# Optimization experiments

Hardware: AMD Instinct MI355X
Metric: run time of the kernel (lower is better)

## Reference

```python
import jax, jax.numpy as jnp
import numpy as np

N_ITERS = 10
LAMBDA0 = 0.01


def skew(p):
    # p: (..., 3) -> (..., 3, 3) skew-symmetric matrices
    x, y, z = p[..., 0], p[..., 1], p[..., 2]
    O = jnp.zeros_like(x)
    return jnp.stack([O, -z, y, z, O, -x, -y, x, O], -1).reshape(p.shape[:-1] + (3, 3))


def so3exp(w):
    # Rodrigues formula for a single (3,) rotation vector
    theta2 = jnp.sum(w * w)
    theta = jnp.sqrt(theta2 + 1e-24)
    small = theta < 1e-4
    a = jnp.where(small, 1.0 - theta2 / 6.0, jnp.sin(theta) / theta)
    b = jnp.where(small, 0.5 - theta2 / 24.0, (1.0 - jnp.cos(theta)) / (theta2 + 1e-24))
    W = skew(w)
    return jnp.eye(3, dtype=w.dtype) + a * W + b * (W @ W)


def gather_feats(fm, p2, width, height):
    # fm: (C, Hf, Wf); p2: (N, 2) int pixel coords (x, y). Mirrors indexing_ with
    # flipped points: row = floor(y*Hf/height), col = floor(x*Wf/width).
    Hf, Wf = fm.shape[1], fm.shape[2]
    rows = jnp.clip((p2[:, 1] * Hf) // height, 0, Hf - 1)
    cols = jnp.clip((p2[:, 0] * Wf) // width, 0, Wf - 1)
    return fm[:, rows, cols].T  # (N, C)


def project(pts3D, R, t, K):
    p3 = pts3D @ R.T + t                                  # (N, 3) camera frame
    proj = p3 @ K.T
    xy = jnp.clip(proj[:, :2] / proj[:, 2:3], -1e6, 1e6)  # from_homogeneous
    p2 = jnp.round(xy).astype(jnp.int32) - 1              # (N, 2) int pixels
    return p3, p2


def support_mask(p2, width, height):
    return (p2[:, 0] >= 0) & (p2[:, 1] >= 0) & (p2[:, 0] < width) & (p2[:, 1] < height)


def masked_mean_cost(fm, feature_ref, p2, mask, width, height):
    err = gather_feats(fm, p2, width, height) - feature_ref
    m = mask.astype(err.dtype)
    c = 0.5 * jnp.sum(err * err, -1) * m
    return jnp.sum(c) / jnp.maximum(jnp.sum(m), 1.0)


def setup_inputs():
    key = jax.random.key(0)
    ks = jax.random.split(key, 7)
    N, C, Hf, Wf = 50000, 128, 480, 640
    z = jax.random.uniform(ks[0], (N,), minval=4.0, maxval=8.0)
    x = jax.random.uniform(ks[1], (N,), minval=-0.4, maxval=0.4) * z
    y = jax.random.uniform(ks[2], (N,), minval=-0.3, maxval=0.3) * z
    pts3D = jnp.stack([x, y, z], -1).astype(jnp.float32)
    feature_map_query = jax.random.normal(ks[3], (C, Hf, Wf), jnp.float32)
    feature_grad_x = 0.1 * jax.random.normal(ks[4], (C, Hf, Wf), jnp.float32)
    feature_grad_y = 0.1 * jax.random.normal(ks[5], (C, Hf, Wf), jnp.float32)
    feature_ref = jax.random.normal(ks[6], (N, C), jnp.float32)
    K = jnp.array([[600.0, 0.0, 320.0], [0.0, 600.0, 240.0], [0.0, 0.0, 1.0]], jnp.float32)
    R_init = jnp.eye(3, dtype=jnp.float32)
    t_init = jnp.array([0.1, 0.1, 0.0], jnp.float32)
    return dict(pts3D=pts3D, feature_ref=feature_ref, feature_map_query=feature_map_query,
                feature_grad_x=feature_grad_x, feature_grad_y=feature_grad_y, K=K,
                R_init=R_init, t_init=t_init, im_width=640, im_height=480)


def reference(pts3D, feature_ref, feature_map_query, feature_grad_x, feature_grad_y,
              K, R_init, t_init, im_width, im_height):
    N = pts3D.shape[0]
    fx, fy = K[0, 0], K[1, 1]
    R, t = R_init, t_init
    lam = jnp.asarray(LAMBDA0, pts3D.dtype)
    lr = jnp.asarray(1.0, pts3D.dtype)
    lr_reset = 1.0

    # initial cost (prev_cost at iteration 0 in the original)
    _, p2_0 = project(pts3D, R, t, K)
    mask0 = support_mask(p2_0, im_width, im_height)
    prev_cost = masked_mean_cost(feature_map_query, feature_ref, p2_0, mask0, im_width, im_height)

    eyeN = jnp.broadcast_to(jnp.eye(3, dtype=pts3D.dtype), (N, 3, 3))

    for _ in range(N_ITERS):
        p3, p2 = project(pts3D, R, t, K)
        mask = support_mask(p2, im_width, im_height)
        m = mask.astype(pts3D.dtype)

        err = gather_feats(feature_map_query, p2, im_width, im_height) - feature_ref  # (N, C)

        Z = p3[:, 2]
        Zs = jnp.where(jnp.abs(Z) > 1e-6, Z, 1e-6)  # guard masked-out points only
        # J_p_T: d p3 / d [t, w]  -> (N, 3, 6)
        J_p_T = jnp.concatenate([eyeN, -skew(p3)], -1)
        o = jnp.ones_like(Zs)
        zz = jnp.zeros_like(Zs)
        # J_px_p: d pixel / d p3 -> (N, 2, 3)
        J_px_p = jnp.stack([fx * o, zz, -fx * p3[:, 0] / Zs,
                            zz, fy * o, -fy * p3[:, 1] / Zs], -1).reshape(N, 2, 3) / Zs[:, None, None]
        gx = gather_feats(feature_grad_x, p2, im_width, im_height)  # (N, C)
        gy = gather_feats(feature_grad_y, p2, im_width, im_height)
        J_f_px = jnp.stack([gx, gy], -1)            # (N, C, 2)
        J = J_f_px @ (J_px_p @ J_p_T)               # (N, C, 6)
        Jm = J * m[:, None, None]                   # zero out unsupported points

        Grad = jnp.einsum('ncj,nc->j', Jm, err)     # (6,)
        Hess = jnp.einsum('nck,ncl->kl', Jm, Jm)    # (6, 6)

        Hd = Hess + lam * jnp.diag(jnp.diagonal(Hess) + 1e-9)
        delta = -lr * (jnp.linalg.inv(Hd) @ Grad)
        dt, dw = delta[:3], delta[3:6]
        dr = so3exp(dw)
        R_new = dr @ R
        t_new = dr @ t + dt

        _, p2n = project(pts3D, R_new, t_new, K)
        maskn = support_mask(p2n, im_width, im_height)
        new_cost = masked_mean_cost(feature_map_query, feature_ref, p2n, maskn, im_width, im_height)

        accept = new_cost <= prev_cost
        lam = jnp.clip(lam * jnp.where(accept, 0.1, 10.0), 1e-6, 1e4)
        lr = jnp.where(accept, lr_reset, jnp.clip(0.1 * lr, 1e-3, 1.0))
        R = jnp.where(accept, R_new, R)
        t = jnp.where(accept, t_new, t)
        prev_cost = jnp.where(accept, new_cost, prev_cost)

    return R, t
```

## Files before the change

### kernel.cpp

```cpp
#include <hip/hip_runtime.h>
#include <math.h>

#define NCH 128
#define IMW 640
#define IMH 480
#define HW (IMW * IMH)
#define THREADS 512
#define WPB (THREADS / 64)
#define GBLK 512
#define TSTRIDE (3 * NCH)

#define S_R    0
#define S_T    9
#define S_RC   12
#define S_TC   21
#define S_LAM  24
#define S_LR   25
#define S_PREV 26
#define S_G    32
#define S_TOTAL 64

#define PCOLS 29

__device__ __forceinline__ float sel6(int k, float v0, float v1, float v2,
                                      float v3, float v4, float v5) {
  float r = v0;
  r = (k == 1) ? v1 : r;
  r = (k == 2) ? v2 : r;
  r = (k == 3) ? v3 : r;
  r = (k == 4) ? v4 : r;
  r = (k == 5) ? v5 : r;
  return r;
}

struct ProjR {
  float x, y, z;
  int pix;
  bool m;
};

__device__ __forceinline__ ProjR project_pt(const float* __restrict__ pts, int n,
                                            const float R[9], const float T[3],
                                            const float Kv[9]) {
  float px = pts[3 * n + 0], py = pts[3 * n + 1], pz = pts[3 * n + 2];
  ProjR o;
  o.x = R[0] * px + R[1] * py + R[2] * pz + T[0];
  o.y = R[3] * px + R[4] * py + R[5] * pz + T[1];
  o.z = R[6] * px + R[7] * py + R[8] * pz + T[2];
  float pr0 = Kv[0] * o.x + Kv[1] * o.y + Kv[2] * o.z;
  float pr1 = Kv[3] * o.x + Kv[4] * o.y + Kv[5] * o.z;
  float pr2 = Kv[6] * o.x + Kv[7] * o.y + Kv[8] * o.z;
  float u = fminf(fmaxf(pr0 / pr2, -1000000.0f), 1000000.0f);
  float v = fminf(fmaxf(pr1 / pr2, -1000000.0f), 1000000.0f);
  int p2x = (int)rintf(u) - 1;
  int p2y = (int)rintf(v) - 1;
  o.m = (p2x >= 0) && (p2y >= 0) && (p2x < IMW) && (p2y < IMH);
  int r = min(max(p2y, 0), IMH - 1);
  int c = min(max(p2x, 0), IMW - 1);
  o.pix = r * IMW + c;
  return o;
}

__device__ __forceinline__ void jac_rows(const ProjR& p, float fx, float fy,
                                         float A0[6], float A1[6]) {
  float Zs = (fabsf(p.z) > 1e-6f) ? p.z : 1e-6f;
  float iz = 1.0f / Zs;
  float j00 = fx * iz;
  float j02 = -fx * p.x * iz * iz;
  float j11 = fy * iz;
  float j12 = -fy * p.y * iz * iz;
  A0[0] = j00; A0[1] = 0.0f; A0[2] = j02;
  A0[3] = j02 * p.y; A0[4] = j00 * p.z - j02 * p.x; A0[5] = -j00 * p.y;
  A1[0] = 0.0f; A1[1] = j11; A1[2] = j12;
  A1[3] = -j11 * p.z + j12 * p.y; A1[4] = -j12 * p.x; A1[5] = j11 * p.x;
}

__global__ void init_kernel(const float* __restrict__ Rin,
                            const float* __restrict__ tin,
                            double* __restrict__ st) {
  int i = threadIdx.x;
  if (i < 9) { st[S_R + i] = (double)Rin[i]; st[S_RC + i] = (double)Rin[i]; }
  if (i < 3) { st[S_T + i] = (double)tin[i]; st[S_TC + i] = (double)tin[i]; }
  if (i == 0) { st[S_LAM] = 0.01; st[S_LR] = 1.0; st[S_PREV] = 0.0; }
}

__global__ __launch_bounds__(256) void transpose3_kernel(
    const float* __restrict__ f, const float* __restrict__ gx,
    const float* __restrict__ gy, float* __restrict__ t) {
  __shared__ float tile[64][NCH + 1];
  const int map = blockIdx.y;
  const float* in = (map == 0) ? f : (map == 1) ? gx : gy;
  const int pix0 = blockIdx.x * 64;
  for (int k = threadIdx.x; k < 64 * NCH / 4; k += 256) {
    int c = k >> 4;
    int p4 = (k & 15) * 4;
    float4 v = ((const float4*)(in + (size_t)c * HW + pix0))[k & 15];
    tile[p4 + 0][c] = v.x;
    tile[p4 + 1][c] = v.y;
    tile[p4 + 2][c] = v.z;
    tile[p4 + 3][c] = v.w;
  }
  __syncthreads();
  for (int k = threadIdx.x; k < 64 * NCH / 4; k += 256) {
    int px = k >> 5;
    int c4 = (k & 31) * 4;
    float4 v = make_float4(tile[px][c4], tile[px][c4 + 1], tile[px][c4 + 2],
                           tile[px][c4 + 3]);
    ((float4*)(t + (size_t)(pix0 + px) * TSTRIDE + (size_t)map * NCH))[k & 31] = v;
  }
}

template <bool TRANS>
__global__ __launch_bounds__(THREADS) void fused_kernel(
    const float* __restrict__ pts, const float* __restrict__ fref,
    const float* __restrict__ mf, const float* __restrict__ mgx,
    const float* __restrict__ mgy, const float* __restrict__ Kmat,
    const double* __restrict__ st, double* __restrict__ part, int N) {
  const int lane = threadIdx.x & 63;
  const int wib = threadIdx.x >> 6;
  const int gw = blockIdx.x * WPB + wib;
  const int nw = gridDim.x * WPB;

  float R[9], T[3], Kv[9];
#pragma unroll
  for (int i = 0; i < 9; ++i) { R[i] = (float)st[S_RC + i]; Kv[i] = Kmat[i]; }
#pragma unroll
  for (int i = 0; i < 3; ++i) T[i] = (float)st[S_TC + i];
  const float fx = Kv[0], fy = Kv[4];

  int kq = 0, lq = 0;
  if (lane < 6) {
    kq = lane; lq = lane;
  } else if (lane < 27) {
    int q = lane - 6, k = 0;
    while (q >= 6 - k) { q -= 6 - k; ++k; }
    kq = k; lq = k + q;
  }

  double acc = 0.0, csum = 0.0, cnt = 0.0;

  for (int n = gw; n < N; n += nw) {
    ProjR p = project_pt(pts, n, R, T, Kv);
    if (!p.m) continue;
    float A0[6], A1[6];
    jac_rows(p, fx, fy, A0, A1);

    float e0, e1, gx0, gx1, gy0, gy1;
    if (TRANS) {
      const size_t base = (size_t)p.pix * TSTRIDE + 2 * lane;
      float2 f  = *(const float2*)(mf + base);
      float2 gx = *(const float2*)(mf + base + NCH);
      float2 gy = *(const float2*)(mf + base + 2 * NCH);
      float2 fr = *(const float2*)(fref + (size_t)n * NCH + 2 * lane);
      e0 = f.x - fr.x; e1 = f.y - fr.y;
      gx0 = gx.x; gx1 = gx.y; gy0 = gy.x; gy1 = gy.y;
    } else {
      const size_t base = (size_t)p.pix;
      const int c0 = lane, c1 = lane + 64;
      float f0 = mf[(size_t)c0 * HW + base], f1 = mf[(size_t)c1 * HW + base];
      gx0 = mgx[(size_t)c0 * HW + base]; gx1 = mgx[(size_t)c1 * HW + base];
      gy0 = mgy[(size_t)c0 * HW + base]; gy1 = mgy[(size_t)c1 * HW + base];
      float r0 = fref[(size_t)n * NCH + c0], r1 = fref[(size_t)n * NCH + c1];
      e0 = f0 - r0; e1 = f1 - r1;
    }

    csum += (double)(e0 * e0 + e1 * e1);
    if (lane == 0) cnt += 1.0;

    float sxx = gx0 * gx0 + gx1 * gx1;
    float sxy = gx0 * gy0 + gx1 * gy1;
    float syy = gy0 * gy0 + gy1 * gy1;
    float sxe = gx0 * e0 + gx1 * e1;
    float sye = gy0 * e0 + gy1 * e1;
#pragma unroll
    for (int off = 32; off > 0; off >>= 1) {
      sxx += __shfl_xor(sxx, off);
      sxy += __shfl_xor(sxy, off);
      syy += __shfl_xor(syy, off);
      sxe += __shfl_xor(sxe, off);
      sye += __shfl_xor(sye, off);
    }
    float a0k = sel6(kq, A0[0], A0[1], A0[2], A0[3], A0[4], A0[5]);
    float a1k = sel6(kq, A1[0], A1[1], A1[2], A1[3], A1[4], A1[5]);
    float a0l = sel6(lq, A0[0], A0[1], A0[2], A0[3], A0[4], A0[5]);
    float a1l = sel6(lq, A1[0], A1[1], A1[2], A1[3], A1[4], A1[5]);
    float contrib;
    if (lane < 6)
      contrib = sxe * a0k + sye * a1k;
    else
      contrib = sxx * a0k * a0l + sxy * (a0k * a1l + a1k * a0l) +
                syy * a1k * a1l;
    if (lane < 27) acc += (double)contrib;
  }

#pragma unroll
  for (int off = 32; off > 0; off >>= 1) {
    csum += __shfl_xor(csum, off);
    cnt += __shfl_xor(cnt, off);
  }

  __shared__ double red[WPB][PCOLS];
  if (lane < 27) red[wib][lane] = acc;
  if (lane == 0) { red[wib][27] = csum; red[wib][28] = cnt; }
  __syncthreads();
  if (wib == 0 && lane < PCOLS) {
    double s = 0.0;
#pragma unroll
    for (int w = 0; w < WPB; ++w) s += red[w][lane];
    part[(size_t)blockIdx.x * PCOLS + lane] = s;
  }
}

__global__ void update_solve_kernel(const double* __restrict__ part, int GB,
                                    double* __restrict__ st,
                                    float* __restrict__ out, int is_init) {
  __shared__ double red[16][PCOLS];
  __shared__ double tot[PCOLS];
  int q = threadIdx.x & 31;
  int chunk = threadIdx.x >> 5;
  if (q < PCOLS) {
    double s = 0.0;
    for (int b = chunk; b < GB; b += 16) s += part[(size_t)b * PCOLS + q];
    red[chunk][q] = s;
  }
  __syncthreads();
  if (threadIdx.x < PCOLS) {
    double t = 0.0;
#pragma unroll
    for (int ch = 0; ch < 16; ++ch) t += red[ch][threadIdx.x];
    tot[threadIdx.x] = t;
  }
  __syncthreads();
  if (threadIdx.x == 0) {
    double nc = 0.5 * tot[27] / fmax(tot[28], 1.0);
    bool accept;
    if (is_init) {
      accept = true;
      st[S_PREV] = nc;
    } else {
      accept = (nc <= st[S_PREV]);
      double lam = st[S_LAM] * (accept ? 0.1 : 10.0);
      st[S_LAM] = fmin(fmax(lam, 1e-6), 1e4);
      st[S_LR] = accept ? 1.0 : fmin(fmax(0.1 * st[S_LR], 1e-3), 1.0);
      if (accept) st[S_PREV] = nc;
    }
    if (accept) {
      for (int i = 0; i < 9; ++i) st[S_R + i] = st[S_RC + i];
      for (int i = 0; i < 3; ++i) st[S_T + i] = st[S_TC + i];
      for (int j = 0; j < 27; ++j) st[S_G + j] = tot[j];
    }
    for (int i = 0; i < 9; ++i) out[i] = (float)st[S_R + i];
    for (int i = 0; i < 3; ++i) out[9 + i] = (float)st[S_T + i];

    double Grad[6], Hs[6][6];
    for (int j = 0; j < 6; ++j) Grad[j] = st[S_G + j];
    int qq = 0;
    for (int k = 0; k < 6; ++k)
      for (int l = k; l < 6; ++l) { Hs[k][l] = Hs[l][k] = st[S_G + 6 + qq]; ++qq; }
    double lam = st[S_LAM], lr = st[S_LR];
    double M[6][7];
    for (int i = 0; i < 6; ++i) {
      for (int j = 0; j < 6; ++j) M[i][j] = Hs[i][j];
      M[i][i] += lam * (Hs[i][i] + 1e-9);
      M[i][6] = Grad[i];
    }
    for (int c = 0; c < 6; ++c) {
      int piv = c;
      double mx = fabs(M[c][c]);
      for (int r = c + 1; r < 6; ++r) {
        double a = fabs(M[r][c]);
        if (a > mx) { mx = a; piv = r; }
      }
      if (piv != c)
        for (int j = 0; j < 7; ++j) {
          double tmp = M[c][j]; M[c][j] = M[piv][j]; M[piv][j] = tmp;
        }
      double pv = M[c][c];
      if (pv == 0.0) pv = 1e-30;
      for (int r = c + 1; r < 6; ++r) {
        double f = M[r][c] / pv;
        for (int j = c; j < 7; ++j) M[r][j] -= f * M[c][j];
      }
    }
    double xs[6];
    for (int i = 5; i >= 0; --i) {
      double v = M[i][6];
      for (int j = i + 1; j < 6; ++j) v -= M[i][j] * xs[j];
      double pv = M[i][i];
      if (pv == 0.0) pv = 1e-30;
      xs[i] = v / pv;
    }
    double dt[3] = {-lr * xs[0], -lr * xs[1], -lr * xs[2]};
    double dw[3] = {-lr * xs[3], -lr * xs[4], -lr * xs[5]};
    double th2 = dw[0] * dw[0] + dw[1] * dw[1] + dw[2] * dw[2];
    double th = sqrt(th2 + 1e-24);
    double a, b;
    if (th < 1e-4) { a = 1.0 - th2 / 6.0; b = 0.5 - th2 / 24.0; }
    else { a = sin(th) / th; b = (1.0 - cos(th)) / (th2 + 1e-24); }
    double W[3][3] = {{0, -dw[2], dw[1]}, {dw[2], 0, -dw[0]}, {-dw[1], dw[0], 0}};
    double W2[3][3];
    for (int i = 0; i < 3; ++i)
      for (int j = 0; j < 3; ++j) {
        double s = 0.0;
        for (int k = 0; k < 3; ++k) s += W[i][k] * W[k][j];
        W2[i][j] = s;
      }
    double dr[3][3];
    for (int i = 0; i < 3; ++i)
      for (int j = 0; j < 3; ++j)
        dr[i][j] = ((i == j) ? 1.0 : 0.0) + a * W[i][j] + b * W2[i][j];
    for (int i = 0; i < 3; ++i) {
      for (int j = 0; j < 3; ++j) {
        double s = 0.0;
        for (int k = 0; k < 3; ++k) s += dr[i][k] * st[S_R + k * 3 + j];
        st[S_RC + i * 3 + j] = s;
      }
      double s = 0.0;
      for (int k = 0; k < 3; ++k) s += dr[i][k] * st[S_T + k];
      st[S_TC + i] = s + dt[i];
    }
  }
}

extern "C" void kernel_launch(void* const* d_in, const int* in_sizes, int n_in,
                              void* d_out, int out_size, void* d_ws, size_t ws_size,
                              hipStream_t stream) {
  const float* pts  = (const float*)d_in[0];
  const float* fref = (const float*)d_in[1];
  const float* fm   = (const float*)d_in[2];
  const float* gxm  = (const float*)d_in[3];
  const float* gym  = (const float*)d_in[4];
  const float* Kmat = (const float*)d_in[5];
  const float* Rin  = (const float*)d_in[6];
  const float* tin  = (const float*)d_in[7];
  const int N = in_sizes[0] / 3;

  double* st = (double*)d_ws;
  double* part = st + S_TOTAL;
  float* out = (float*)d_out;

  const size_t state_doubles = S_TOTAL + (size_t)GBLK * PCOLS;
  const size_t map_floats = (size_t)HW * NCH;
  const size_t need_fast =
      state_doubles * sizeof(double) + 3 * map_floats * sizeof(float) + 256;

  init_kernel<<<1, 64, 0, stream>>>(Rin, tin, st);

  if (ws_size >= need_fast) {
    float* tmap = (float*)(st + state_doubles);
    transpose3_kernel<<<dim3(HW / 64, 3), 256, 0, stream>>>(fm, gxm, gym, tmap);
    fused_kernel<true><<<GBLK, THREADS, 0, stream>>>(pts, fref, tmap, tmap, tmap,
                                                     Kmat, st, part, N);
    update_solve_kernel<<<1, 512, 0, stream>>>(part, GBLK, st, out, 1);
    for (int it = 0; it < 10; ++it) {
      fused_kernel<true><<<GBLK, THREADS, 0, stream>>>(pts, fref, tmap, tmap,
                                                       tmap, Kmat, st, part, N);
      update_solve_kernel<<<1, 512, 0, stream>>>(part, GBLK, st, out, 0);
    }
  } else {
    fused_kernel<false><<<GBLK, THREADS, 0, stream>>>(pts, fref, fm, gxm, gym,
                                                      Kmat, st, part, N);
    update_solve_kernel<<<1, 512, 0, stream>>>(part, GBLK, st, out, 1);
    for (int it = 0; it < 10; ++it) {
      fused_kernel<false><<<GBLK, THREADS, 0, stream>>>(pts, fref, fm, gxm, gym,
                                                        Kmat, st, part, N);
      update_solve_kernel<<<1, 512, 0, stream>>>(part, GBLK, st, out, 0);
    }
  }
}
```

Baseline: 957.6 us.

## Process two points per wavefront with float4 loads and per-lane Hessian accumulators

The fused Gauss-Newton kernel now handles two points per 64-lane wavefront, one per half-wave, with each lane loading float4 channel chunks. Each lane keeps all 27 Hessian and gradient terms in float registers and reduces them once after the loop, which removes the per-point cross-lane shuffle reductions and the sel6 selects. The transpose kernel switches to an XOR-swizzled float4 shared-memory tile with unrolled loops to avoid bank conflicts. The cost is higher register pressure from the 27 accumulators and float rather than double accumulation for the Hessian inside each lane.

```diff
diff --git a/kernel.cpp b/kernel.cpp
--- a/kernel.cpp
+++ b/kernel.cpp
@@ -21,17 +21,6 @@
 #define S_TOTAL 64
 
 #define PCOLS 29
-
-__device__ __forceinline__ float sel6(int k, float v0, float v1, float v2,
-                                      float v3, float v4, float v5) {
-  float r = v0;
-  r = (k == 1) ? v1 : r;
-  r = (k == 2) ? v2 : r;
-  r = (k == 3) ? v3 : r;
-  r = (k == 4) ? v4 : r;
-  r = (k == 5) ? v5 : r;
-  return r;
-}
 
 struct ProjR {
   float x, y, z;
@@ -87,26 +76,31 @@
 __global__ __launch_bounds__(256) void transpose3_kernel(
     const float* __restrict__ f, const float* __restrict__ gx,
     const float* __restrict__ gy, float* __restrict__ t) {
-  __shared__ float tile[64][NCH + 1];
+  __shared__ float4 tile4[64][32];
   const int map = blockIdx.y;
   const float* in = (map == 0) ? f : (map == 1) ? gx : gy;
   const int pix0 = blockIdx.x * 64;
-  for (int k = threadIdx.x; k < 64 * NCH / 4; k += 256) {
-    int c = k >> 4;
+#pragma unroll
+  for (int mm = 0; mm < 8; ++mm) {
+    int k = threadIdx.x + 256 * mm;
+    int c  = k >> 4;
     int p4 = (k & 15) * 4;
     float4 v = ((const float4*)(in + (size_t)c * HW + pix0))[k & 15];
-    tile[p4 + 0][c] = v.x;
-    tile[p4 + 1][c] = v.y;
-    tile[p4 + 2][c] = v.z;
-    tile[p4 + 3][c] = v.w;
+    int sw = (c >> 2) ^ (k & 15);
+    int e  = c & 3;
+    ((float*)&tile4[p4 + 0][sw])[e] = v.x;
+    ((float*)&tile4[p4 + 1][sw])[e] = v.y;
+    ((float*)&tile4[p4 + 2][sw])[e] = v.z;
+    ((float*)&tile4[p4 + 3][sw])[e] = v.w;
   }
   __syncthreads();
-  for (int k = threadIdx.x; k < 64 * NCH / 4; k += 256) {
+#pragma unroll
+  for (int mm = 0; mm < 8; ++mm) {
+    int k = threadIdx.x + 256 * mm;
     int px = k >> 5;
-    int c4 = (k & 31) * 4;
-    float4 v = make_float4(tile[px][c4], tile[px][c4 + 1], tile[px][c4 + 2],
-                           tile[px][c4 + 3]);
-    ((float4*)(t + (size_t)(pix0 + px) * TSTRIDE + (size_t)map * NCH))[k & 31] = v;
+    int c4 = k & 31;
+    float4 v = tile4[px][c4 ^ (px >> 2)];
+    ((float4*)(t + (size_t)(pix0 + px) * TSTRIDE + (size_t)map * NCH))[c4] = v;
   }
 }
 
@@ -117,9 +111,11 @@
     const float* __restrict__ mgy, const float* __restrict__ Kmat,
     const double* __restrict__ st, double* __restrict__ part, int N) {
   const int lane = threadIdx.x & 63;
-  const int wib = threadIdx.x >> 6;
+  const int wib  = threadIdx.x >> 6;
   const int gw = blockIdx.x * WPB + wib;
   const int nw = gridDim.x * WPB;
+  const int half = lane >> 5;
+  const int hl   = lane & 31;
 
   float R[9], T[3], Kv[9];
 #pragma unroll
@@ -128,80 +124,101 @@
   for (int i = 0; i < 3; ++i) T[i] = (float)st[S_TC + i];
   const float fx = Kv[0], fy = Kv[4];
 
-  int kq = 0, lq = 0;
-  if (lane < 6) {
-    kq = lane; lq = lane;
-  } else if (lane < 27) {
-    int q = lane - 6, k = 0;
-    while (q >= 6 - k) { q -= 6 - k; ++k; }
-    kq = k; lq = k + q;
-  }
-
-  double acc = 0.0, csum = 0.0, cnt = 0.0;
-
-  for (int n = gw; n < N; n += nw) {
-    ProjR p = project_pt(pts, n, R, T, Kv);
-    if (!p.m) continue;
+  float hacc[27];
+#pragma unroll
+  for (int j = 0; j < 27; ++j) hacc[j] = 0.0f;
+  double csum = 0.0;
+  float cntf = 0.0f;
+
+  for (int base = gw * 2; base < N; base += 2 * nw) {
+    const int n = base + half;
+    const int nc = min(n, N - 1);
+    ProjR p = project_pt(pts, nc, R, T, Kv);
+    const float m = (p.m && n < N) ? 1.0f : 0.0f;
+    if (__all(m == 0.0f)) continue;
+
     float A0[6], A1[6];
     jac_rows(p, fx, fy, A0, A1);
 
-    float e0, e1, gx0, gx1, gy0, gy1;
+    float e0, e1, e2, e3;
+    float gxx, gxy, gyy, gxe, gye;
     if (TRANS) {
-      const size_t base = (size_t)p.pix * TSTRIDE + 2 * lane;
-      float2 f  = *(const float2*)(mf + base);
-      float2 gx = *(const float2*)(mf + base + NCH);
-      float2 gy = *(const float2*)(mf + base + 2 * NCH);
-      float2 fr = *(const float2*)(fref + (size_t)n * NCH + 2 * lane);
-      e0 = f.x - fr.x; e1 = f.y - fr.y;
-      gx0 = gx.x; gx1 = gx.y; gy0 = gy.x; gy1 = gy.y;
+      const float4* t4 = (const float4*)mf;
+      const size_t b = (size_t)p.pix * (TSTRIDE / 4) + hl;
+      float4 fv = t4[b];
+      float4 gv = t4[b + 32];
+      float4 hv = t4[b + 64];
+      float4 rv = ((const float4*)fref)[(size_t)nc * (NCH / 4) + hl];
+      e0 = fv.x - rv.x; e1 = fv.y - rv.y; e2 = fv.z - rv.z; e3 = fv.w - rv.w;
+      gxx = gv.x * gv.x + gv.y * gv.y + gv.z * gv.z + gv.w * gv.w;
+      gxy = gv.x * hv.x + gv.y * hv.y + gv.z * hv.z + gv.w * hv.w;
+      gyy = hv.x * hv.x + hv.y * hv.y + hv.z * hv.z + hv.w * hv.w;
+      gxe = gv.x * e0 + gv.y * e1 + gv.z * e2 + gv.w * e3;
+      gye = hv.x * e0 + hv.y * e1 + hv.z * e2 + hv.w * e3;
     } else {
-      const size_t base = (size_t)p.pix;
-      const int c0 = lane, c1 = lane + 64;
-      float f0 = mf[(size_t)c0 * HW + base], f1 = mf[(size_t)c1 * HW + base];
-      gx0 = mgx[(size_t)c0 * HW + base]; gx1 = mgx[(size_t)c1 * HW + base];
-      gy0 = mgy[(size_t)c0 * HW + base]; gy1 = mgy[(size_t)c1 * HW + base];
-      float r0 = fref[(size_t)n * NCH + c0], r1 = fref[(size_t)n * NCH + c1];
-      e0 = f0 - r0; e1 = f1 - r1;
-    }
-
-    csum += (double)(e0 * e0 + e1 * e1);
-    if (lane == 0) cnt += 1.0;
-
-    float sxx = gx0 * gx0 + gx1 * gx1;
-    float sxy = gx0 * gy0 + gx1 * gy1;
-    float syy = gy0 * gy0 + gy1 * gy1;
-    float sxe = gx0 * e0 + gx1 * e1;
-    float sye = gy0 * e0 + gy1 * e1;
+      const int c0 = hl * 4;
+      const size_t bb = (size_t)p.pix;
+      float f0 = mf[(size_t)(c0 + 0) * HW + bb];
+      float f1 = mf[(size_t)(c0 + 1) * HW + bb];
+      float f2 = mf[(size_t)(c0 + 2) * HW + bb];
+      float f3 = mf[(size_t)(c0 + 3) * HW + bb];
+      float gx0 = mgx[(size_t)(c0 + 0) * HW + bb];
+      float gx1 = mgx[(size_t)(c0 + 1) * HW + bb];
+      float gx2 = mgx[(size_t)(c0 + 2) * HW + bb];
+      float gx3 = mgx[(size_t)(c0 + 3) * HW + bb];
+      float gy0 = mgy[(size_t)(c0 + 0) * HW + bb];
+      float gy1 = mgy[(size_t)(c0 + 1) * HW + bb];
+      float gy2 = mgy[(size_t)(c0 + 2) * HW + bb];
+      float gy3 = mgy[(size_t)(c0 + 3) * HW + bb];
+      float4 rv = ((const float4*)fref)[(size_t)nc * (NCH / 4) + hl];
+      e0 = f0 - rv.x; e1 = f1 - rv.y; e2 = f2 - rv.z; e3 = f3 - rv.w;
+      gxx = gx0 * gx0 + gx1 * gx1 + gx2 * gx2 + gx3 * gx3;
+      gxy = gx0 * gy0 + gx1 * gy1 + gx2 * gy2 + gx3 * gy3;
+      gyy = gy0 * gy0 + gy1 * gy1 + gy2 * gy2 + gy3 * gy3;
+      gxe = gx0 * e0 + gx1 * e1 + gx2 * e2 + gx3 * e3;
+      gye = gy0 * e0 + gy1 * e1 + gy2 * e2 + gy3 * e3;
+    }
+
+    gxx *= m; gxy *= m; gyy *= m; gxe *= m; gye *= m;
+    csum += (double)(m * (e0 * e0 + e1 * e1 + e2 * e2 + e3 * e3));
+    if (hl == 0) cntf += m;
+
+#pragma unroll
+    for (int k = 0; k < 6; ++k) hacc[k] += gxe * A0[k] + gye * A1[k];
+    float u[6], v[6];
+#pragma unroll
+    for (int k = 0; k < 6; ++k) {
+      u[k] = gxx * A0[k] + gxy * A1[k];
+      v[k] = gxy * A0[k] + gyy * A1[k];
+    }
+    int q = 6;
+#pragma unroll
+    for (int k = 0; k < 6; ++k)
+#pragma unroll
+      for (int l = k; l < 6; ++l) {
+        hacc[q] += u[k] * A0[l] + v[k] * A1[l];
+        ++q;
+      }
+  }
+
+  __shared__ double red[WPB][PCOLS];
+#pragma unroll
+  for (int j = 0; j < 27; ++j) {
+    double d = (double)hacc[j];
+#pragma unroll
+    for (int off = 32; off > 0; off >>= 1) d += __shfl_xor(d, off);
+    if (lane == 0) red[wib][j] = d;
+  }
+  {
+    double cs = csum;
+    float cf = cntf;
 #pragma unroll
     for (int off = 32; off > 0; off >>= 1) {
-      sxx += __shfl_xor(sxx, off);
-      sxy += __shfl_xor(sxy, off);
-      syy += __shfl_xor(syy, off);
-      sxe += __shfl_xor(sxe, off);
-      sye += __shfl_xor(sye, off);
-    }
-    float a0k = sel6(kq, A0[0], A0[1], A0[2], A0[3], A0[4], A0[5]);
-    float a1k = sel6(kq, A1[0], A1[1], A1[2], A1[3], A1[4], A1[5]);
-    float a0l = sel6(lq, A0[0], A0[1], A0[2], A0[3], A0[4], A0[5]);
-    float a1l = sel6(lq, A1[0], A1[1], A1[2], A1[3], A1[4], A1[5]);
-    float contrib;
-    if (lane < 6)
-      contrib = sxe * a0k + sye * a1k;
-    else
-      contrib = sxx * a0k * a0l + sxy * (a0k * a1l + a1k * a0l) +
-                syy * a1k * a1l;
-    if (lane < 27) acc += (double)contrib;
-  }
-
-#pragma unroll
-  for (int off = 32; off > 0; off >>= 1) {
-    csum += __shfl_xor(csum, off);
-    cnt += __shfl_xor(cnt, off);
-  }
-
-  __shared__ double red[WPB][PCOLS];
-  if (lane < 27) red[wib][lane] = acc;
-  if (lane == 0) { red[wib][27] = csum; red[wib][28] = cnt; }
+      cs += __shfl_xor(cs, off);
+      cf += __shfl_xor(cf, off);
+    }
+    if (lane == 0) { red[wib][27] = cs; red[wib][28] = (double)cf; }
+  }
   __syncthreads();
   if (wib == 0 && lane < PCOLS) {
     double s = 0.0;
```

After: 1.033 ms. +7.9%, slower.

## Sort points by initial projected pixel bucket and retile the feature-map transpose

Applied to the files above, without the earlier changes.

Adds a counting sort of the points by their initial projected pixel (in buckets of 64 pixels) and permutes the points and reference features into that order. Later gathers from the transposed feature maps then hit nearby memory. The transpose kernel is also rewritten to use 32-pixel tiles, 512 threads, all three maps per block, and a swizzled float4 shared layout to avoid bank conflicts. In exchange it adds five extra kernels, an atomic scatter and more workspace. The locality gain relies on the pose staying close to the initial one across iterations.

```diff
diff --git a/kernel.cpp b/kernel.cpp
--- a/kernel.cpp
+++ b/kernel.cpp
@@ -9,6 +9,9 @@
 #define WPB (THREADS / 64)
 #define GBLK 512
 #define TSTRIDE (3 * NCH)
+#define TPX 32
+#define NTILE (HW / TPX)
+#define NBUCK (HW / 64)
 
 #define S_R    0
 #define S_T    9
@@ -77,36 +80,131 @@
 
 __global__ void init_kernel(const float* __restrict__ Rin,
                             const float* __restrict__ tin,
-                            double* __restrict__ st) {
-  int i = threadIdx.x;
-  if (i < 9) { st[S_R + i] = (double)Rin[i]; st[S_RC + i] = (double)Rin[i]; }
-  if (i < 3) { st[S_T + i] = (double)tin[i]; st[S_TC + i] = (double)tin[i]; }
-  if (i == 0) { st[S_LAM] = 0.01; st[S_LR] = 1.0; st[S_PREV] = 0.0; }
-}
-
-__global__ __launch_bounds__(256) void transpose3_kernel(
+                            double* __restrict__ st, int* __restrict__ hist) {
+  if (blockIdx.x == 0) {
+    int i = threadIdx.x;
+    if (i < 9) { st[S_R + i] = (double)Rin[i]; st[S_RC + i] = (double)Rin[i]; }
+    if (i < 3) { st[S_T + i] = (double)tin[i]; st[S_TC + i] = (double)tin[i]; }
+    if (i == 0) { st[S_LAM] = 0.01; st[S_LR] = 1.0; st[S_PREV] = 0.0; }
+  }
+  int gid = blockIdx.x * blockDim.x + threadIdx.x;
+  for (int i = gid; i < NBUCK; i += gridDim.x * blockDim.x) hist[i] = 0;
+}
+
+__global__ __launch_bounds__(256) void sort_key_kernel(
+    const float* __restrict__ pts, const float* __restrict__ Rin,
+    const float* __restrict__ tin, const float* __restrict__ Kmat,
+    int* __restrict__ keys, int* __restrict__ hist, int N) {
+  int n = blockIdx.x * 256 + threadIdx.x;
+  if (n >= N) return;
+  float R[9], T[3], Kv[9];
+#pragma unroll
+  for (int i = 0; i < 9; ++i) { R[i] = Rin[i]; Kv[i] = Kmat[i]; }
+#pragma unroll
+  for (int i = 0; i < 3; ++i) T[i] = tin[i];
+  ProjR p = project_pt(pts, n, R, T, Kv);
+  keys[n] = p.pix;
+  atomicAdd(&hist[p.pix >> 6], 1);
+}
+
+__global__ __launch_bounds__(512) void sort_scan_kernel(
+    const int* __restrict__ hist, int* __restrict__ offs) {
+  __shared__ int tsum[512];
+  const int C = (NBUCK + 511) / 512;
+  int t = threadIdx.x;
+  int local[C];
+  int s = 0;
+#pragma unroll
+  for (int j = 0; j < C; ++j) {
+    int idx = t * C + j;
+    int v = (idx < NBUCK) ? hist[idx] : 0;
+    local[j] = s;
+    s += v;
+  }
+  tsum[t] = s;
+  __syncthreads();
+  for (int off = 1; off < 512; off <<= 1) {
+    int y = (t >= off) ? tsum[t - off] : 0;
+    __syncthreads();
+    tsum[t] += y;
+    __syncthreads();
+  }
+  int base = (t == 0) ? 0 : tsum[t - 1];
+#pragma unroll
+  for (int j = 0; j < C; ++j) {
+    int idx = t * C + j;
+    if (idx < NBUCK) offs[idx] = base + local[j];
+  }
+}
+
+__global__ __launch_bounds__(256) void sort_scatter_kernel(
+    const int* __restrict__ keys, int* __restrict__ offs,
+    int* __restrict__ order, int N) {
+  int n = blockIdx.x * 256 + threadIdx.x;
+  if (n >= N) return;
+  int b = keys[n] >> 6;
+  int pos = atomicAdd(&offs[b], 1);
+  order[pos] = n;
+}
+
+__global__ __launch_bounds__(256) void permute_kernel(
+    const float* __restrict__ pts, const float* __restrict__ fref,
+    const int* __restrict__ order, float* __restrict__ pts_s,
+    float* __restrict__ fref_s, int N) {
+  int gid = blockIdx.x * 256 + threadIdx.x;
+  int tot4 = N * (NCH / 4);
+  for (int idx = gid; idx < tot4; idx += gridDim.x * 256) {
+    int i = idx >> 5, c4 = idx & 31;
+    int n = order[i];
+    ((float4*)fref_s)[(size_t)i * 32 + c4] =
+        ((const float4*)fref)[(size_t)n * 32 + c4];
+  }
+  int tot3 = N * 3;
+  for (int idx = gid; idx < tot3; idx += gridDim.x * 256) {
+    int i = idx / 3, r = idx - i * 3;
+    pts_s[idx] = pts[3 * order[i] + r];
+  }
+}
+
+__global__ __launch_bounds__(512) void transpose3_kernel(
     const float* __restrict__ f, const float* __restrict__ gx,
     const float* __restrict__ gy, float* __restrict__ t) {
-  __shared__ float tile[64][NCH + 1];
-  const int map = blockIdx.y;
-  const float* in = (map == 0) ? f : (map == 1) ? gx : gy;
-  const int pix0 = blockIdx.x * 64;
-  for (int k = threadIdx.x; k < 64 * NCH / 4; k += 256) {
-    int c = k >> 4;
-    int p4 = (k & 15) * 4;
-    float4 v = ((const float4*)(in + (size_t)c * HW + pix0))[k & 15];
-    tile[p4 + 0][c] = v.x;
-    tile[p4 + 1][c] = v.y;
-    tile[p4 + 2][c] = v.z;
-    tile[p4 + 3][c] = v.w;
+  __shared__ float4 l4[TPX * 96];
+  const int bx = blockIdx.x;
+  const int tile = (bx & 7) * (NTILE / 8) + (bx >> 3);
+  const int pix0 = tile * TPX;
+
+  float4 v[6];
+#pragma unroll
+  for (int it = 0; it < 6; ++it) {
+    int k = threadIdx.x + 512 * it;
+    int map = k >> 10;
+    int r = k & 1023;
+    int c = r >> 3;
+    int g = r & 7;
+    const float* in = (map == 0) ? f : (map == 1) ? gx : gy;
+    v[it] = ((const float4*)(in + (size_t)c * HW + pix0))[g];
+  }
+#pragma unroll
+  for (int it = 0; it < 6; ++it) {
+    int k = threadIdx.x + 512 * it;
+    int map = k >> 10;
+    int r = k & 1023;
+    int c = r >> 3, g = r & 7;
+    int j = map * 32 + (c >> 2), e = c & 3;
+    int jb = j ^ g;
+    ((float*)&l4[(4 * g + 0) * 96 + (jb ^ 0)])[e] = v[it].x;
+    ((float*)&l4[(4 * g + 1) * 96 + (jb ^ 1)])[e] = v[it].y;
+    ((float*)&l4[(4 * g + 2) * 96 + (jb ^ 2)])[e] = v[it].z;
+    ((float*)&l4[(4 * g + 3) * 96 + (jb ^ 3)])[e] = v[it].w;
   }
   __syncthreads();
-  for (int k = threadIdx.x; k < 64 * NCH / 4; k += 256) {
-    int px = k >> 5;
-    int c4 = (k & 31) * 4;
-    float4 v = make_float4(tile[px][c4], tile[px][c4 + 1], tile[px][c4 + 2],
-                           tile[px][c4 + 3]);
-    ((float4*)(t + (size_t)(pix0 + px) * TSTRIDE + (size_t)map * NCH))[k & 31] = v;
+#pragma unroll
+  for (int it = 0; it < 6; ++it) {
+    int o = threadIdx.x + 512 * it;
+    int px = o / 96, j = o % 96;
+    float4 w = l4[px * 96 + (j ^ ((px >> 2) & 7) ^ (px & 3))];
+    ((float4*)t)[(size_t)pix0 * 96 + o] = w;
   }
 }
 
@@ -337,20 +435,48 @@
 
   double* st = (double*)d_ws;
   double* part = st + S_TOTAL;
+  int* keys  = (int*)(part + (size_t)GBLK * PCOLS);
+  int* order = keys + N;
+  int* hist  = order + N;
+  int* offs  = hist + NBUCK;
+  size_t int_end = (size_t)((char*)(offs + NBUCK) - (char*)d_ws);
+
+  const size_t map_floats = (size_t)HW * NCH;
+
+  size_t pts_off  = (int_end + 15) & ~(size_t)15;
+  size_t fref_off = (pts_off + (size_t)3 * N * 4 + 15) & ~(size_t)15;
+  size_t tmap_s_off = (fref_off + (size_t)N * NCH * 4 + 15) & ~(size_t)15;
+  const size_t need_sorted = tmap_s_off + 3 * map_floats * 4 + 256;
+  size_t tmap_p_off = (int_end + 15) & ~(size_t)15;
+  const size_t need_plain = tmap_p_off + 3 * map_floats * 4 + 256;
+
   float* out = (float*)d_out;
 
-  const size_t state_doubles = S_TOTAL + (size_t)GBLK * PCOLS;
-  const size_t map_floats = (size_t)HW * NCH;
-  const size_t need_fast =
-      state_doubles * sizeof(double) + 3 * map_floats * sizeof(float) + 256;
-
-  init_kernel<<<1, 64, 0, stream>>>(Rin, tin, st);
-
-  if (ws_size >= need_fast) {
-    float* tmap = (float*)(st + state_doubles);
-    transpose3_kernel<<<dim3(HW / 64, 3), 256, 0, stream>>>(fm, gxm, gym, tmap);
-    fused_kernel<true><<<GBLK, THREADS, 0, stream>>>(pts, fref, tmap, tmap, tmap,
-                                                     Kmat, st, part, N);
+  init_kernel<<<10, 512, 0, stream>>>(Rin, tin, st, hist);
+
+  if (ws_size >= need_sorted) {
+    float* pts_s  = (float*)((char*)d_ws + pts_off);
+    float* fref_s = (float*)((char*)d_ws + fref_off);
+    float* tmap   = (float*)((char*)d_ws + tmap_s_off);
+    const int npb = (N + 255) / 256;
+    sort_key_kernel<<<npb, 256, 0, stream>>>(pts, Rin, tin, Kmat, keys, hist, N);
+    sort_scan_kernel<<<1, 512, 0, stream>>>(hist, offs);
+    sort_scatter_kernel<<<npb, 256, 0, stream>>>(keys, offs, order, N);
+    permute_kernel<<<1024, 256, 0, stream>>>(pts, fref, order, pts_s, fref_s, N);
+    transpose3_kernel<<<NTILE, 512, 0, stream>>>(fm, gxm, gym, tmap);
+    fused_kernel<true><<<GBLK, THREADS, 0, stream>>>(pts_s, fref_s, tmap, tmap,
+                                                     tmap, Kmat, st, part, N);
+    update_solve_kernel<<<1, 512, 0, stream>>>(part, GBLK, st, out, 1);
+    for (int it = 0; it < 10; ++it) {
+      fused_kernel<true><<<GBLK, THREADS, 0, stream>>>(pts_s, fref_s, tmap, tmap,
+                                                       tmap, Kmat, st, part, N);
+      update_solve_kernel<<<1, 512, 0, stream>>>(part, GBLK, st, out, 0);
+    }
+  } else if (ws_size >= need_plain) {
+    float* tmap = (float*)((char*)d_ws + tmap_p_off);
+    transpose3_kernel<<<NTILE, 512, 0, stream>>>(fm, gxm, gym, tmap);
+    fused_kernel<true><<<GBLK, THREADS, 0, stream>>>(pts, fref, tmap, tmap,
+                                                     tmap, Kmat, st, part, N);
     update_solve_kernel<<<1, 512, 0, stream>>>(part, GBLK, st, out, 1);
     for (int it = 0; it < 10; ++it) {
       fused_kernel<true><<<GBLK, THREADS, 0, stream>>>(pts, fref, tmap, tmap,
```

New measurement: 974.0 us. Within noise of the previous version (+1.7%).
